# Kernel optimization log

Hardware: AMD Instinct MI355X
Metric: run time of the kernel (lower is better)

The kernel has to match this reference:

```python
import jax, jax.numpy as jnp
import numpy as np

EPS = 1e-6

def elu_feature_map(x):
    return jax.nn.elu(x) + 1.0

def setup_inputs() -> dict:
    key = jax.random.key(0)
    kq, kk, kv = jax.random.split(key, 3)
    N, L, S, H, D = 8, 8192, 8192, 8, 32
    queries = jax.random.normal(kq, (N, L, H, D), dtype=jnp.float32)
    keys = jax.random.normal(kk, (N, S, H, D), dtype=jnp.float32)
    values = jax.random.normal(kv, (N, S, H, D), dtype=jnp.float32)
    return {"queries": queries, "keys": keys, "values": values}

def reference(queries, keys, values):
    # Linear attention ("Transformers are RNNs"), ELU+1 feature map.
    Q = elu_feature_map(queries)            # [N, L, H, D]
    K = elu_feature_map(keys)               # [N, S, H, D]
    v_length = values.shape[1]
    v = values / v_length                   # [N, S, H, D]
    # KV = sum_s K_s (outer) V_s  -> [N, H, D, D] (fused, no per-token outer products)
    KV = jnp.einsum('nshd,nshv->nhdv', K, v)
    # Normalizer: Z = 1 / (Q . sum_s K_s + eps)  -> [N, L, H]
    K_sum = K.sum(axis=1)                   # [N, H, D]
    Z = 1.0 / (jnp.einsum('nlhd,nhd->nlh', Q, K_sum) + EPS)
    # out = (Q @ KV) * Z * v_length  -> [N, L, H, D]
    out = jnp.einsum('nlhd,nhdv->nlhv', Q, KV) * Z[..., None] * v_length
    return out
```

## Files before the change

### kernel.cpp

```cpp
#include <hip/hip_runtime.h>


#define NN 8
#define LL 8192
#define SS 8192
#define HH 8
#define DD 32
#define HD 256
#define EPSF 1e-6f

#define KV_FLOATS (NN*HH*DD*DD)
#define FINAL_FLOATS (KV_FLOATS + NN*HH*DD)

#define P1_CHUNKS 64
#define P1_BLOCKS (NN*P1_CHUNKS)
#define P1_CS (SS/P1_CHUNKS)
#define P1_TS 16
#define PBLK 8448

#define P2_I 128
#define P2_BLOCKS (NN*4*(LL/P2_I))

__device__ __forceinline__ float elu1(float x) {
    return x > 0.f ? x + 1.f : __expf(x);
}
#define ELU4(v) { v.x = elu1(v.x); v.y = elu1(v.y); v.z = elu1(v.z); v.w = elu1(v.w); }

template<bool ATOMIC>
__global__ __launch_bounds__(256)
void la_phase1(const float* __restrict__ keys, const float* __restrict__ values,
               float* __restrict__ outbuf) {
    __shared__ float4 lK4[P1_TS*64];
    __shared__ float4 lV4[P1_TS*64];
    const int t = threadIdx.x;
    const int b = blockIdx.x;
    const int n = b / P1_CHUNKS;
    const int s0 = (b % P1_CHUNKS) * P1_CS;
    const int h  = t >> 5;
    const int dO = (t >> 3) & 3;
    const int vO = t & 7;

    const float4* Kg = (const float4*)(keys   + ((size_t)n*SS + s0)*HD);
    const float4* Vg = (const float4*)(values + ((size_t)n*SS + s0)*HD);

    float4 acc[8];
#pragma unroll
    for (int i = 0; i < 8; ++i) acc[i] = make_float4(0.f,0.f,0.f,0.f);
    float4 ksa = make_float4(0.f,0.f,0.f,0.f), ksb = make_float4(0.f,0.f,0.f,0.f);

    float4 kp[4], vp[4];
#pragma unroll
    for (int r = 0; r < 4; ++r) { kp[r] = Kg[t + 256*r]; vp[r] = Vg[t + 256*r]; }

    const int kbase = h*8 + dO*2;
    const int vbase = h*8 + vO;

    for (int si = 0; si < P1_CS; si += P1_TS) {
#pragma unroll
        for (int r = 0; r < 4; ++r) ELU4(kp[r]);
        __syncthreads();
#pragma unroll
        for (int r = 0; r < 4; ++r) { lK4[t + 256*r] = kp[r]; lV4[t + 256*r] = vp[r]; }
        __syncthreads();
        if (si + P1_TS < P1_CS) {
            const int nb = (si + P1_TS) * 64;
#pragma unroll
            for (int r = 0; r < 4; ++r) { kp[r] = Kg[nb + t + 256*r]; vp[r] = Vg[nb + t + 256*r]; }
        }
#pragma unroll
        for (int i = 0; i < P1_TS; ++i) {
            const float4 k0 = lK4[i*64 + kbase];
            const float4 k1 = lK4[i*64 + kbase + 1];
            const float4 vv = lV4[i*64 + vbase];
            ksa.x += k0.x; ksa.y += k0.y; ksa.z += k0.z; ksa.w += k0.w;
            ksb.x += k1.x; ksb.y += k1.y; ksb.z += k1.z; ksb.w += k1.w;
#define P1F(A,S) A.x=fmaf(S,vv.x,A.x); A.y=fmaf(S,vv.y,A.y); A.z=fmaf(S,vv.z,A.z); A.w=fmaf(S,vv.w,A.w);
            P1F(acc[0],k0.x) P1F(acc[1],k0.y) P1F(acc[2],k0.z) P1F(acc[3],k0.w)
            P1F(acc[4],k1.x) P1F(acc[5],k1.y) P1F(acc[6],k1.z) P1F(acc[7],k1.w)
#undef P1F
        }
    }

    if (ATOMIC) {
        float* kvb = outbuf + (size_t)n*(HH*DD*DD) + h*(DD*DD) + (dO*8)*DD + vO*4;
#pragma unroll
        for (int dd = 0; dd < 8; ++dd) {
            atomicAdd(kvb + dd*DD + 0, acc[dd].x);
            atomicAdd(kvb + dd*DD + 1, acc[dd].y);
            atomicAdd(kvb + dd*DD + 2, acc[dd].z);
            atomicAdd(kvb + dd*DD + 3, acc[dd].w);
        }
        if (vO == 0) {
            float* kb = outbuf + KV_FLOATS + n*HD + h*DD + dO*8;
            atomicAdd(kb+0, ksa.x); atomicAdd(kb+1, ksa.y); atomicAdd(kb+2, ksa.z); atomicAdd(kb+3, ksa.w);
            atomicAdd(kb+4, ksb.x); atomicAdd(kb+5, ksb.y); atomicAdd(kb+6, ksb.z); atomicAdd(kb+7, ksb.w);
        }
    } else {
        float4* pb4 = (float4*)(outbuf + (size_t)b * PBLK);
#pragma unroll
        for (int dd = 0; dd < 8; ++dd) pb4[h*256 + (dO*8+dd)*8 + vO] = acc[dd];
        if (vO == 0) { pb4[2048 + h*8 + dO*2] = ksa; pb4[2048 + h*8 + dO*2 + 1] = ksb; }
    }
}

__global__ __launch_bounds__(256)
void la_reduce(const float* __restrict__ part, float* __restrict__ finalbuf) {
    const int o = blockIdx.x * 256 + threadIdx.x;
    const int n = o / PBLK;
    const int e = o - n * PBLK;
    const float* p = part + (size_t)(n * P1_CHUNKS) * PBLK + e;
    float s = 0.f;
#pragma unroll 8
    for (int c = 0; c < P1_CHUNKS; ++c) s += p[(size_t)c * PBLK];
    if (e < HH*DD*DD) finalbuf[(size_t)n*(HH*DD*DD) + e] = s;
    else              finalbuf[KV_FLOATS + n*HD + (e - HH*DD*DD)] = s;
}

__global__ __launch_bounds__(256)
void la_phase2(const float* __restrict__ queries, const float* __restrict__ finalbuf,
               float* __restrict__ out) {
    __shared__ float4 lqt4s[2*DD*P2_I/4];
    __shared__ float4 lkv4[2*DD*DD/4];
    __shared__ float4 lks4[16];
    float* lqt = (float*)lqt4s;

    const int t = threadIdx.x;
    const int b = blockIdx.x;
    const int n  = b >> 8;
    const int hp = (b >> 6) & 3;
    const int l0 = (b & 63) * P2_I;

    const float4* fin4 = (const float4*)finalbuf;
    lkv4[t]       = fin4[(size_t)n*2048 + hp*512 + t];
    lkv4[t + 256] = fin4[(size_t)n*2048 + hp*512 + t + 256];
    if (t < 16) lks4[t] = fin4[KV_FLOATS/4 + n*64 + hp*16 + t];

    const int irow = t >> 4;
    const int shh  = (t >> 3) & 1;
    const int d4   = t & 7;
    const float4* Qg4 = (const float4*)queries;
    const size_t qb = ((size_t)n*LL + l0)*64 + (size_t)(hp*16 + shh*8 + d4);
    float* dst0 = lqt + shh*4096 + (d4*4)*P2_I;
#pragma unroll
    for (int k = 0; k < 8; ++k) {
        const int i = irow + k*16;
        float4 qv = Qg4[qb + (size_t)i*64];
        ELU4(qv);
        const int ip = i ^ (d4 << 2);
        dst0[ip] = qv.x; dst0[P2_I + ip] = qv.y; dst0[2*P2_I + ip] = qv.z; dst0[3*P2_I + ip] = qv.w;
    }
    __syncthreads();

    const int voct = t & 3;
    const int hh   = (t >> 2) & 1;
    const int lq   = t >> 3;

    float4 a0[4], a1[4];
#pragma unroll
    for (int i = 0; i < 4; ++i) { a0[i] = make_float4(0.f,0.f,0.f,0.f); a1[i] = make_float4(0.f,0.f,0.f,0.f); }
    float z0 = 0.f, z1 = 0.f, z2 = 0.f, z3 = 0.f;

    const float4* lqt4 = (const float4*)lqt;
    const int qbase  = hh*1024;
    const int kvbase = hh*256 + voct*2;

#define FMA8(L, QS) \
    a0[L].x = fmaf(QS, kA.x, a0[L].x); a0[L].y = fmaf(QS, kA.y, a0[L].y); \
    a0[L].z = fmaf(QS, kA.z, a0[L].z); a0[L].w = fmaf(QS, kA.w, a0[L].w); \
    a1[L].x = fmaf(QS, kB.x, a1[L].x); a1[L].y = fmaf(QS, kB.y, a1[L].y); \
    a1[L].z = fmaf(QS, kB.z, a1[L].z); a1[L].w = fmaf(QS, kB.w, a1[L].w);

#define P2S(J, KSD) { \
    const int d = dq*4 + (J); \
    const float4 qv = lqt4[qbase + d*32 + (lq ^ dq)]; \
    const float4 kA = lkv4[kvbase + d*8]; \
    const float4 kB = lkv4[kvbase + d*8 + 1]; \
    z0 = fmaf(qv.x, KSD, z0); z1 = fmaf(qv.y, KSD, z1); \
    z2 = fmaf(qv.z, KSD, z2); z3 = fmaf(qv.w, KSD, z3); \
    FMA8(0, qv.x) FMA8(1, qv.y) FMA8(2, qv.z) FMA8(3, qv.w) }

#pragma unroll
    for (int dq = 0; dq < 8; ++dq) {
        const float4 ks = lks4[hh*8 + dq];
        P2S(0, ks.x) P2S(1, ks.y) P2S(2, ks.z) P2S(3, ks.w)
    }
#undef P2S
#undef FMA8

    float4* out4 = (float4*)out;
    const size_t ob = ((size_t)n*LL + l0 + lq*4)*64 + (size_t)(hp*16 + hh*8 + voct*2);
#define P2OUT(L, ZV) { \
    const float zi = 1.0f/((ZV) + EPSF); \
    float4 r0 = a0[L], r1 = a1[L]; \
    r0.x*=zi; r0.y*=zi; r0.z*=zi; r0.w*=zi; r1.x*=zi; r1.y*=zi; r1.z*=zi; r1.w*=zi; \
    out4[ob + (size_t)(L)*64] = r0; out4[ob + (size_t)(L)*64 + 1] = r1; }
    P2OUT(0, z0) P2OUT(1, z1) P2OUT(2, z2) P2OUT(3, z3)
#undef P2OUT
}

extern "C" void kernel_launch(void* const* d_in, const int* in_sizes, int n_in,
                              void* d_out, int out_size, void* d_ws, size_t ws_size,
                              hipStream_t stream) {
    const float* q = (const float*)d_in[0];
    const float* k = (const float*)d_in[1];
    const float* v = (const float*)d_in[2];
    float* out = (float*)d_out;

    const size_t partial_floats = (size_t)P1_BLOCKS * PBLK;
    const size_t need = (partial_floats + FINAL_FLOATS) * sizeof(float);

    if (ws_size >= need) {
        float* part = (float*)d_ws;
        float* fin  = part + partial_floats;
        la_phase1<false><<<dim3(P1_BLOCKS), dim3(256), 0, stream>>>(k, v, part);
        la_reduce<<<dim3(FINAL_FLOATS/256), dim3(256), 0, stream>>>(part, fin);
        la_phase2<<<dim3(P2_BLOCKS), dim3(256), 0, stream>>>(q, fin, out);
    } else {
        float* fin = (float*)d_ws;
        hipMemsetAsync(fin, 0, FINAL_FLOATS*sizeof(float), stream);
        la_phase1<true><<<dim3(P1_BLOCKS), dim3(256), 0, stream>>>(k, v, fin);
        la_phase2<<<dim3(P2_BLOCKS), dim3(256), 0, stream>>>(q, fin, out);
    }
}
```

Before: 242.9 us.

## Double-buffer phase1 LDS tiles with one barrier per step and more chunks

Phase 1 now uses a double-buffered shared-memory tile, so the next tile is written to the alternate buffer while the current one is computed, needing one barrier per step instead of two. The sequence is also split into 128 chunks of 64 tokens (up from 64 chunks of 128) with 8-token tiles, doubling the block count for more parallelism. The cost is twice as many partial buffers, so the reduce kernel reads more data. However, PBLK and the reduce sizing stay fixed while the partial buffer count doubles, and the reduce still loops over P1_CHUNKS, so this is consistent.

Result: slower. 270.1 us (+11.2%).

```diff
diff --git a/kernel.cpp b/kernel.cpp
--- a/kernel.cpp
+++ b/kernel.cpp
@@ -12,10 +12,11 @@
 #define KV_FLOATS (NN*HH*DD*DD)
 #define FINAL_FLOATS (KV_FLOATS + NN*HH*DD)
 
-#define P1_CHUNKS 64
+#define P1_CHUNKS 128
 #define P1_BLOCKS (NN*P1_CHUNKS)
-#define P1_CS (SS/P1_CHUNKS)
-#define P1_TS 16
+#define P1_CS 64
+#define P1_TS 8
+#define P1_NT (P1_CS/P1_TS)
 #define PBLK 8448
 
 #define P2_I 128
@@ -30,8 +31,7 @@
 __global__ __launch_bounds__(256)
 void la_phase1(const float* __restrict__ keys, const float* __restrict__ values,
                float* __restrict__ outbuf) {
-    __shared__ float4 lK4[P1_TS*64];
-    __shared__ float4 lV4[P1_TS*64];
+    __shared__ float4 lbuf4[2048];
     const int t = threadIdx.x;
     const int b = blockIdx.x;
     const int n = b / P1_CHUNKS;
@@ -48,47 +48,71 @@
     for (int i = 0; i < 8; ++i) acc[i] = make_float4(0.f,0.f,0.f,0.f);
     float4 ksa = make_float4(0.f,0.f,0.f,0.f), ksb = make_float4(0.f,0.f,0.f,0.f);
 
-    float4 kp[4], vp[4];
-#pragma unroll
-    for (int r = 0; r < 4; ++r) { kp[r] = Kg[t + 256*r]; vp[r] = Vg[t + 256*r]; }
-
     const int kbase = h*8 + dO*2;
     const int vbase = h*8 + vO;
 
-    for (int si = 0; si < P1_CS; si += P1_TS) {
-#pragma unroll
-        for (int r = 0; r < 4; ++r) ELU4(kp[r]);
+    float4 ka0 = Kg[t], ka1 = Kg[t+256], va0 = Vg[t], va1 = Vg[t+256];
+    float4 kb0 = Kg[512+t], kb1 = Kg[512+t+256], vb0 = Vg[512+t], vb1 = Vg[512+t+256];
+    ELU4(ka0); ELU4(ka1);
+    lbuf4[t] = ka0; lbuf4[t+256] = ka1;
+    lbuf4[512+t] = va0; lbuf4[512+t+256] = va1;
+    __syncthreads();
+
+#define P1_COMPUTE(P) { \
+    const float4* lK4 = lbuf4 + (P)*1024; \
+    const float4* lV4 = lK4 + 512; \
+    _Pragma("unroll") \
+    for (int i = 0; i < P1_TS; ++i) { \
+        const float4 k0 = lK4[i*64 + kbase]; \
+        const float4 k1 = lK4[i*64 + kbase + 1]; \
+        const float4 vv = lV4[i*64 + vbase]; \
+        ksa.x += k0.x; ksa.y += k0.y; ksa.z += k0.z; ksa.w += k0.w; \
+        ksb.x += k1.x; ksb.y += k1.y; ksb.z += k1.z; ksb.w += k1.w; \
+        acc[0].x=fmaf(k0.x,vv.x,acc[0].x); acc[0].y=fmaf(k0.x,vv.y,acc[0].y); \
+        acc[0].z=fmaf(k0.x,vv.z,acc[0].z); acc[0].w=fmaf(k0.x,vv.w,acc[0].w); \
+        acc[1].x=fmaf(k0.y,vv.x,acc[1].x); acc[1].y=fmaf(k0.y,vv.y,acc[1].y); \
+        acc[1].z=fmaf(k0.y,vv.z,acc[1].z); acc[1].w=fmaf(k0.y,vv.w,acc[1].w); \
+        acc[2].x=fmaf(k0.z,vv.x,acc[2].x); acc[2].y=fmaf(k0.z,vv.y,acc[2].y); \
+        acc[2].z=fmaf(k0.z,vv.z,acc[2].z); acc[2].w=fmaf(k0.z,vv.w,acc[2].w); \
+        acc[3].x=fmaf(k0.w,vv.x,acc[3].x); acc[3].y=fmaf(k0.w,vv.y,acc[3].y); \
+        acc[3].z=fmaf(k0.w,vv.z,acc[3].z); acc[3].w=fmaf(k0.w,vv.w,acc[3].w); \
+        acc[4].x=fmaf(k1.x,vv.x,acc[4].x); acc[4].y=fmaf(k1.x,vv.y,acc[4].y); \
+        acc[4].z=fmaf(k1.x,vv.z,acc[4].z); acc[4].w=fmaf(k1.x,vv.w,acc[4].w); \
+        acc[5].x=fmaf(k1.y,vv.x,acc[5].x); acc[5].y=fmaf(k1.y,vv.y,acc[5].y); \
+        acc[5].z=fmaf(k1.y,vv.z,acc[5].z); acc[5].w=fmaf(k1.y,vv.w,acc[5].w); \
+        acc[6].x=fmaf(k1.z,vv.x,acc[6].x); acc[6].y=fmaf(k1.z,vv.y,acc[6].y); \
+        acc[6].z=fmaf(k1.z,vv.z,acc[6].z); acc[6].w=fmaf(k1.z,vv.w,acc[6].w); \
+        acc[7].x=fmaf(k1.w,vv.x,acc[7].x); acc[7].y=fmaf(k1.w,vv.y,acc[7].y); \
+        acc[7].z=fmaf(k1.w,vv.z,acc[7].z); acc[7].w=fmaf(k1.w,vv.w,acc[7].w); \
+    } }
+
+#pragma unroll
+    for (int st = 0; st < P1_NT - 1; ++st) {
+        const int wp = (st + 1) & 1;
+        ELU4(kb0); ELU4(kb1);
+        float4* wb = lbuf4 + wp*1024;
+        wb[t] = kb0; wb[t+256] = kb1;
+        wb[512+t] = vb0; wb[512+t+256] = vb1;
+        if (st + 2 < P1_NT) {
+            const int off = (st + 2) * 512;
+            kb0 = Kg[off+t]; kb1 = Kg[off+t+256];
+            vb0 = Vg[off+t]; vb1 = Vg[off+t+256];
+        }
+        P1_COMPUTE(st & 1)
         __syncthreads();
-#pragma unroll
-        for (int r = 0; r < 4; ++r) { lK4[t + 256*r] = kp[r]; lV4[t + 256*r] = vp[r]; }
-        __syncthreads();
-        if (si + P1_TS < P1_CS) {
-            const int nb = (si + P1_TS) * 64;
-#pragma unroll
-            for (int r = 0; r < 4; ++r) { kp[r] = Kg[nb + t + 256*r]; vp[r] = Vg[nb + t + 256*r]; }
-        }
-#pragma unroll
-        for (int i = 0; i < P1_TS; ++i) {
-            const float4 k0 = lK4[i*64 + kbase];
-            const float4 k1 = lK4[i*64 + kbase + 1];
-            const float4 vv = lV4[i*64 + vbase];
-            ksa.x += k0.x; ksa.y += k0.y; ksa.z += k0.z; ksa.w += k0.w;
-            ksb.x += k1.x; ksb.y += k1.y; ksb.z += k1.z; ksb.w += k1.w;
-#define P1F(A,S) A.x=fmaf(S,vv.x,A.x); A.y=fmaf(S,vv.y,A.y); A.z=fmaf(S,vv.z,A.z); A.w=fmaf(S,vv.w,A.w);
-            P1F(acc[0],k0.x) P1F(acc[1],k0.y) P1F(acc[2],k0.z) P1F(acc[3],k0.w)
-            P1F(acc[4],k1.x) P1F(acc[5],k1.y) P1F(acc[6],k1.z) P1F(acc[7],k1.w)
-#undef P1F
-        }
-    }
+    }
+    P1_COMPUTE((P1_NT - 1) & 1)
+#undef P1_COMPUTE
 
     if (ATOMIC) {
         float* kvb = outbuf + (size_t)n*(HH*DD*DD) + h*(DD*DD) + (dO*8)*DD + vO*4;
 #pragma unroll
         for (int dd = 0; dd < 8; ++dd) {
-            atomicAdd(kvb + dd*DD + 0, acc[dd].x);
-            atomicAdd(kvb + dd*DD + 1, acc[dd].y);
-            atomicAdd(kvb + dd*DD + 2, acc[dd].z);
-            atomicAdd(kvb + dd*DD + 3, acc[dd].w);
+            const float4 a = acc[dd];
+            atomicAdd(kvb + dd*DD + 0, a.x);
+            atomicAdd(kvb + dd*DD + 1, a.y);
+            atomicAdd(kvb + dd*DD + 2, a.z);
+            atomicAdd(kvb + dd*DD + 3, a.w);
         }
         if (vO == 0) {
             float* kb = outbuf + KV_FLOATS + n*HD + h*DD + dO*8;
```
